# Kernel tuning notes

Measured on AMD Instinct MI355X. Metric: run time of the kernel, lower is better.

## Reference

```python
import jax, jax.numpy as jnp
import numpy as np

B, T, N = 512, 200, 256
ENC_G, ENC_C = 256, 256
C_DIM, G_DIM, U_DIM, F_DIM = 128, 256, 64, 64
CLIP = 5.0


def _gru(x, h, Wih, Whh, bih, bhh):
    # PyTorch nn.GRUCell math
    gi = x @ Wih.T + bih
    gh = h @ Whh.T + bhh
    ir, iz, inn = jnp.split(gi, 3, axis=-1)
    hr, hz, hn = jnp.split(gh, 3, axis=-1)
    r = jax.nn.sigmoid(ir + hr)
    z = jax.nn.sigmoid(iz + hz)
    n = jnp.tanh(inn + r * hn)
    return (1.0 - z) * n + z * h


def setup_inputs() -> dict:
    key = jax.random.key(0)
    ks = iter(jax.random.split(key, 64))

    def gru_p(i, h):
        return (jax.random.normal(next(ks), (3 * h, i)) * i ** -0.5,
                jax.random.normal(next(ks), (3 * h, h)) * h ** -0.5,
                jnp.zeros(3 * h), jnp.zeros(3 * h))

    def lin_p(i, o):
        return (jax.random.normal(next(ks), (o, i)) * i ** -0.5, jnp.zeros(o))

    inp = {}
    inp['x'] = jax.random.uniform(next(ks), (B, T, N))
    inp['eps_g0'] = jax.random.normal(next(ks), (B, G_DIM))
    inp['eps_u'] = jax.random.normal(next(ks), (B, T, U_DIM))
    for name, (i, h) in [('gf', (N, ENC_G)), ('gb', (N, ENC_G)),
                         ('cf', (N, ENC_C)), ('cb', (N, ENC_C)),
                         ('ct', (2 * ENC_C + F_DIM, C_DIM)), ('gn', (U_DIM, G_DIM))]:
        Wih, Whh, bih, bhh = gru_p(i, h)
        inp['Wih_' + name] = Wih; inp['Whh_' + name] = Whh
        inp['bih_' + name] = bih; inp['bhh_' + name] = bhh
    for name, (i, o) in [('g0m', (2 * ENC_G, G_DIM)), ('g0v', (2 * ENC_G, G_DIM)),
                         ('um', (C_DIM, U_DIM)), ('uv', (C_DIM, U_DIM)),
                         ('f', (G_DIM, F_DIM)), ('r', (F_DIM, N))]:
        W, b = lin_p(i, o)
        inp['W_' + name] = W; inp['b_' + name] = b
    return inp


def reference(x, eps_g0, eps_u,
              Wih_gf, Whh_gf, bih_gf, bhh_gf,
              Wih_gb, Whh_gb, bih_gb, bhh_gb,
              Wih_cf, Whh_cf, bih_cf, bhh_cf,
              Wih_cb, Whh_cb, bih_cb, bhh_cb,
              Wih_ct, Whh_ct, bih_ct, bhh_ct,
              Wih_gn, Whh_gn, bih_gn, bhh_gn,
              W_g0m, b_g0m, W_g0v, b_g0v,
              W_um, b_um, W_uv, b_uv,
              W_f, b_f, W_r, b_r):
    Bsz = x.shape[0]
    xs = x.transpose(1, 0, 2)  # [T, B, N]
    zg = jnp.zeros((Bsz, ENC_G), x.dtype)
    zc = jnp.zeros((Bsz, ENC_C), x.dtype)

    def make_enc(pg, pc):
        def step(carry, xt):
            hg, hc = carry
            hg = jnp.minimum(_gru(xt, hg, *pg), CLIP)   # clamp(max=clip_val)
            hc = jnp.minimum(_gru(xt, hc, *pc), CLIP)
            return (hg, hc), hc
        return step

    (hgf, _), hcf = jax.lax.scan(
        make_enc((Wih_gf, Whh_gf, bih_gf, bhh_gf), (Wih_cf, Whh_cf, bih_cf, bhh_cf)),
        (zg, zc), xs)
    (hgb, _), hcb = jax.lax.scan(
        make_enc((Wih_gb, Whh_gb, bih_gb, bhh_gb), (Wih_cb, Whh_cb, bih_cb, bhh_cb)),
        (zg, zc), xs[::-1])
    h_enc_g = jnp.concatenate([hgf, hgb], axis=-1)        # [B, 2*ENC_G]
    h_enc_c = jnp.concatenate([hcf, hcb[::-1]], axis=-1)  # [T, B, 2*ENC_C]

    g0_mean = h_enc_g @ W_g0m.T + b_g0m
    g0_logv = jnp.log(jnp.exp(h_enc_g @ W_g0v.T + b_g0v) + 1e-4)
    g0 = eps_g0 * jnp.exp(0.5 * g0_logv) + g0_mean

    f0 = g0 @ W_f.T + b_f
    hc0 = jnp.zeros((Bsz, C_DIM), x.dtype)

    def gen_step(carry, inp):
        h_c, g, f = carry
        henc_t, eps_t = inp
        cin = jnp.concatenate([henc_t, f], axis=-1)
        h_c = jnp.clip(_gru(cin, h_c, Wih_ct, Whh_ct, bih_ct, bhh_ct), 0.0, CLIP)
        um = h_c @ W_um.T + b_um
        ul = h_c @ W_uv.T + b_uv
        u = eps_t * jnp.exp(0.5 * ul) + um
        g = jnp.clip(_gru(u, g, Wih_gn, Whh_gn, bih_gn, bhh_gn), 0.0, CLIP)
        f = g @ W_f.T + b_f
        return (h_c, g, f), (um, ul, f)

    _, (u_means, u_logvs, factors) = jax.lax.scan(
        gen_step, (hc0, g0, f0), (h_enc_c, eps_u.transpose(1, 0, 2)))
    factors = factors.transpose(1, 0, 2)  # [B, T, F_DIM]
    rates = jnp.exp(jnp.clip(factors @ W_r.T + b_r, -CLIP, CLIP))
    return (g0_mean, g0_logv,
            u_means.transpose(1, 0, 2), u_logvs.transpose(1, 0, 2),
            factors, rates)
```

## Files before the change

### kernel.cpp

```cpp
#include <hip/hip_runtime.h>
#include <hip/hip_bf16.h>
#include <stdint.h>

typedef __bf16 bf16x8 __attribute__((ext_vector_type(8)));
typedef __bf16 bf16x4 __attribute__((ext_vector_type(4)));
typedef float  f32x4  __attribute__((ext_vector_type(4)));
typedef unsigned short u16x8 __attribute__((ext_vector_type(8)));

#define MFMA_B16(A_,B_,C_) __builtin_amdgcn_mfma_f32_16x16x32_bf16((A_),(B_),(C_),0,0,0)

static constexpr int TT = 200;
static constexpr int TC = 25;
static constexpr int NCH = 8;

static __device__ __forceinline__ float sig_f(float x){ return 1.f/(1.f+__expf(-x)); }
static __device__ __forceinline__ float tanh_f(float x){
  float e = __expf(-2.f*fabsf(x));
  float t = (1.f-e)/(1.f+e);
  return x<0.f ? -t : t;
}
static __device__ __forceinline__ float bf2f(unsigned short u){
  union{unsigned int i; float f;} v; v.i = ((unsigned)u)<<16; return v.f;
}
static __device__ __forceinline__ int swz_off(int row, int col_bytes, int strideB){
  return (row*strideB + col_bytes) ^ ((row&7)<<4);
}
static __device__ __forceinline__ bf16x8 lds_rdA(const __bf16* buf, int row, int kt, int lq, int strideB){
  return *(const bf16x8*)((const char*)buf + swz_off(row, kt*64 + lq*16, strideB));
}
static __device__ __forceinline__ void lds_wr(__bf16* buf, int row, int dim, int strideB, float v){
  *(__bf16*)((char*)buf + swz_off(row, dim*2, strideB)) = (__bf16)v;
}
static __device__ __forceinline__ void lds_barrier(){
  asm volatile("s_waitcnt lgkmcnt(0)" ::: "memory");
  __builtin_amdgcn_s_barrier();
}

__global__ void cvt_bf16(const float* __restrict__ s, __bf16* __restrict__ d, int n){
  int i = blockIdx.x*blockDim.x + threadIdx.x;
  int st = gridDim.x*blockDim.x;
  for(; i<n; i+=st) d[i] = (__bf16)s[i];
}

__global__ __launch_bounds__(256) void gi_gemm(const float* __restrict__ x,
                                               const __bf16* __restrict__ Wall,
                                               __bf16* __restrict__ gi, int t0){
  const int tid=threadIdx.x, w=tid>>6, l=tid&63, lr=l&15, lq=l>>4;
  const int cell = blockIdx.y;
  const bool fwd = (cell&1)==0;
  const int m0 = blockIdx.x*64;
  const int tloc = m0>>9, b0 = m0&511;
  const int tabs = fwd ? (t0+tloc) : (TT-1-(t0+tloc));
  const int brow = b0 + w*16 + lr;

  const float* xp = x + (size_t)brow*TT*256 + (size_t)tabs*256 + lq*8;
  bf16x8 a[8];
  #pragma unroll
  for(int kt=0;kt<8;kt++){
    float4 f0 = *(const float4*)(xp + kt*32);
    float4 f1 = *(const float4*)(xp + kt*32 + 4);
    bf16x8 v;
    v[0]=(__bf16)f0.x; v[1]=(__bf16)f0.y; v[2]=(__bf16)f0.z; v[3]=(__bf16)f0.w;
    v[4]=(__bf16)f1.x; v[5]=(__bf16)f1.y; v[6]=(__bf16)f1.z; v[7]=(__bf16)f1.w;
    a[kt]=v;
  }
  const __bf16* Wc = Wall + (size_t)cell*768*256;
  #pragma unroll 1
  for(int nt=0;nt<48;nt++){
    f32x4 acc={};
    const __bf16* bp = Wc + (size_t)(nt*16+lr)*256 + lq*8;
    #pragma unroll
    for(int kt=0;kt<8;kt++)
      acc = MFMA_B16(a[kt], *(const bf16x8*)(bp + kt*32), acc);
    bf16x4 pk;
    pk[0]=(__bf16)acc[0]; pk[1]=(__bf16)acc[1]; pk[2]=(__bf16)acc[2]; pk[3]=(__bf16)acc[3];
    *(bf16x4*)(gi + (((size_t)cell*TC + tloc)*768 + nt*16+lr)*512 + b0 + w*16 + lq*4) = pk;
  }
}

struct EncP{
  const __bf16* whh;
  const float*  bih[4];
  const float*  bhh[4];
  const __bf16* gi;
  __bf16* henc;
  float*  hcar;
  int t0;
};
__global__ __launch_bounds__(512,2) void enc_scan(EncP P){
  const int tid=threadIdx.x, w=tid>>6, l=tid&63, lr=l&15, lq=l>>4;
  const int cell=blockIdx.y, b0=blockIdx.x*16;
  const bool fwd = (cell&1)==0;
  const bool isC = cell>=2;
  const int dim0 = w*32;

  __shared__ __align__(16) __bf16 hA[2][16*256];
  __shared__ __align__(16) __bf16 giL[2][768*16];
  __shared__ float blds[1024];

  for(int d=tid; d<256; d+=512){
    blds[d]     = P.bih[cell][d]     + P.bhh[cell][d];
    blds[256+d] = P.bih[cell][256+d] + P.bhh[cell][256+d];
    blds[512+d] = P.bih[cell][512+d];
    blds[768+d] = P.bhh[cell][512+d];
  }
  bf16x8 wreg[2][3][8];
  {
    const __bf16* Wh = P.whh + (size_t)cell*768*256;
    #pragma unroll
    for(int jt=0;jt<2;jt++)
      #pragma unroll
      for(int g=0;g<3;g++)
        #pragma unroll
        for(int kt=0;kt<8;kt++)
          wreg[jt][g][kt] = *(const bf16x8*)(Wh + (size_t)(g*256 + dim0 + jt*16 + lr)*256 + kt*32 + lq*8);
  }
  f32x4 hold[2];
  #pragma unroll
  for(int jt=0;jt<2;jt++)
    #pragma unroll
    for(int rr=0;rr<4;rr++){
      float v = P.hcar[((size_t)cell*512 + b0 + lq*4+rr)*256 + dim0 + jt*16 + lr];
      hold[jt][rr] = v;
      lds_wr(hA[0], lq*4+rr, dim0+jt*16+lr, 512, v);
    }
  const int prow = w*96 + (l>>1), phal = l&1;
  const __bf16* gbase = P.gi + ((size_t)cell*TC*768 + prow)*512 + b0 + phal*8;
  u16x8 pf0, pf1, pf2;
  pf0 = *(const u16x8*)(gbase + (size_t)0*768*512 +  0*512);
  pf1 = *(const u16x8*)(gbase + (size_t)0*768*512 + 32*512);
  pf2 = *(const u16x8*)(gbase + (size_t)0*768*512 + 64*512);
  __syncthreads();
  {
    __bf16* gl = giL[0] + prow*16 + phal*8;
    *(u16x8*)(gl)        = pf0;
    *(u16x8*)(gl+32*16)  = pf1;
    *(u16x8*)(gl+64*16)  = pf2;
  }
  { int sn = 1 < TC ? 1 : TC-1;
    pf0 = *(const u16x8*)(gbase + (size_t)sn*768*512 +  0*512);
    pf1 = *(const u16x8*)(gbase + (size_t)sn*768*512 + 32*512);
    pf2 = *(const u16x8*)(gbase + (size_t)sn*768*512 + 64*512);
  }
  lds_barrier();

  int p=0, q=0;
  #pragma unroll 1
  for(int s=0;s<TC;s++){
    const int tglob = P.t0 + s;
    const int tx = fwd ? tglob : (TT-1-tglob);
    if(s+1<TC){
      __bf16* gl = giL[1-q] + prow*16 + phal*8;
      *(u16x8*)(gl)        = pf0;
      *(u16x8*)(gl+32*16)  = pf1;
      *(u16x8*)(gl+64*16)  = pf2;
    }
    { int sn = (s+2<TC) ? s+2 : TC-1;
      pf0 = *(const u16x8*)(gbase + (size_t)sn*768*512 +  0*512);
      pf1 = *(const u16x8*)(gbase + (size_t)sn*768*512 + 32*512);
      pf2 = *(const u16x8*)(gbase + (size_t)sn*768*512 + 64*512);
    }
    const __bf16* gq = giL[q];
    #pragma unroll
    for(int jt=0;jt<2;jt++){
      f32x4 aR={}, aZ={}, aH={};
      #pragma unroll
      for(int kt=0;kt<8;kt++){
        bf16x8 frag = lds_rdA(hA[p], lr, kt, lq, 512);
        aR = MFMA_B16(frag, wreg[jt][0][kt], aR);
        aZ = MFMA_B16(frag, wreg[jt][1][kt], aZ);
        aH = MFMA_B16(frag, wreg[jt][2][kt], aH);
      }
      const int d = dim0 + jt*16 + lr;
      ushort4 gR = *(const ushort4*)(gq + (0*256+d)*16 + lq*4);
      ushort4 gZ = *(const ushort4*)(gq + (1*256+d)*16 + lq*4);
      ushort4 gN = *(const ushort4*)(gq + (2*256+d)*16 + lq*4);
      const float bR=blds[d], bZ=blds[256+d], bI=blds[512+d], bH=blds[768+d];
      const unsigned short* uR=(const unsigned short*)&gR;
      const unsigned short* uZ=(const unsigned short*)&gZ;
      const unsigned short* uN=(const unsigned short*)&gN;
      #pragma unroll
      for(int rr=0;rr<4;rr++){
        float r = sig_f(aR[rr] + bf2f(uR[rr]) + bR);
        float z = sig_f(aZ[rr] + bf2f(uZ[rr]) + bZ);
        float nn= tanh_f(bf2f(uN[rr]) + bI + r*(aH[rr] + bH));
        float h = (1.f-z)*nn + z*hold[jt][rr];
        h = fminf(h, 5.f);
        hold[jt][rr] = h;
        lds_wr(hA[1-p], lq*4+rr, d, 512, h);
      }
    }
    if(isC){
      const int row = l>>2, dgrp = (l&3)*8;
      bf16x8 hv = *(const bf16x8*)((const char*)hA[1-p] +
                    ((row*512 + (dim0+dgrp)*2) ^ ((row&7)<<4)));
      *(bf16x8*)(P.henc + ((size_t)tx*512 + b0 + row)*512 + (cell==3?256:0) + dim0 + dgrp) = hv;
    }
    lds_barrier();
    p ^= 1; q ^= 1;
  }
  #pragma unroll
  for(int jt=0;jt<2;jt++)
    #pragma unroll
    for(int rr=0;rr<4;rr++)
      P.hcar[((size_t)cell*512 + b0 + lq*4+rr)*256 + dim0 + jt*16 + lr] = hold[jt][rr];
}

__global__ void g0_kernel(const float* __restrict__ hgf, const float* __restrict__ hgb,
                          const float* __restrict__ Wm, const float* __restrict__ bm,
                          const float* __restrict__ Wv, const float* __restrict__ bv,
                          const float* __restrict__ eps,
                          float* __restrict__ o_mean, float* __restrict__ o_logv,
                          float* __restrict__ g0){
  int j = blockIdx.x*blockDim.x + threadIdx.x;
  int b = j>>8, d = j&255;
  const float4* hf=(const float4*)(hgf + (size_t)b*256);
  const float4* hb=(const float4*)(hgb + (size_t)b*256);
  const float4* mp=(const float4*)(Wm + (size_t)d*512);
  const float4* vp=(const float4*)(Wv + (size_t)d*512);
  float am=0.f, av=0.f;
  #pragma unroll 4
  for(int k=0;k<64;k++){
    float4 h=hf[k], m=mp[k], v=vp[k];
    am += h.x*m.x + h.y*m.y + h.z*m.z + h.w*m.w;
    av += h.x*v.x + h.y*v.y + h.z*v.z + h.w*v.w;
  }
  #pragma unroll 4
  for(int k=0;k<64;k++){
    float4 h=hb[k], m=mp[64+k], v=vp[64+k];
    am += h.x*m.x + h.y*m.y + h.z*m.z + h.w*m.w;
    av += h.x*v.x + h.y*v.y + h.z*v.z + h.w*v.w;
  }
  float mean = am + bm[d];
  float ev   = __expf(av + bv[d]) + 1e-4f;
  float lv   = __logf(ev);
  o_mean[j]=mean; o_logv[j]=lv;
  g0[j] = eps[j]*sqrtf(ev) + mean;
}

__global__ __launch_bounds__(256,2) void gict_gemm(const __bf16* __restrict__ henc,
                                                   const __bf16* __restrict__ wct,
                                                   __bf16* __restrict__ gictT){
  const int tid=threadIdx.x, w=tid>>6, l=tid&63, lr=l&15, lq=l>>4;
  const int m0 = blockIdx.x*8 + w*2;
  bf16x8 a[2][16];
  #pragma unroll
  for(int m=0;m<2;m++){
    const __bf16* ap = henc + (size_t)((m0+m)*16 + lr)*512 + lq*8;
    #pragma unroll
    for(int kt=0;kt<16;kt++) a[m][kt] = *(const bf16x8*)(ap + kt*32);
  }
  #pragma unroll 1
  for(int nt=0;nt<24;nt++){
    f32x4 c0={}, c1={};
    const __bf16* bp = wct + (size_t)(nt*16+lr)*576 + lq*8;
    #pragma unroll
    for(int kt=0;kt<16;kt++){
      bf16x8 bb = *(const bf16x8*)(bp + kt*32);
      c0 = MFMA_B16(a[0][kt], bb, c0);
      c1 = MFMA_B16(a[1][kt], bb, c1);
    }
    #pragma unroll
    for(int m=0;m<2;m++){
      f32x4 c = m? c1 : c0;
      int R0 = (m0+m)*16 + lq*4;
      int t  = R0>>9, b = R0&511;
      bf16x4 pk;
      pk[0]=(__bf16)c[0]; pk[1]=(__bf16)c[1]; pk[2]=(__bf16)c[2]; pk[3]=(__bf16)c[3];
      *(bf16x4*)(gictT + ((size_t)t*384 + nt*16+lr)*512 + b) = pk;
    }
  }
}

struct GenP{
  const __bf16 *wct, *whh_ct, *wih_gn, *whh_gn, *w_um, *w_uv, *w_f;
  const float  *bih_ct, *bhh_ct, *bih_gn, *bhh_gn, *b_um, *b_uv, *b_f;
  const __bf16* gihT;
  const float*  g0;
  const float*  eps_u;
  float *o_um, *o_ul, *o_f;
};
__global__ __launch_bounds__(512,2) void gen_scan(GenP P){
  const int tid=threadIdx.x, w=tid>>6, l=tid&63, lr=l&15, lq=l>>4;
  const int b0 = blockIdx.x*16;

  __shared__ __align__(16) __bf16 wgnL[768*64];
  __shared__ __align__(16) __bf16 hcA[2][16*128];
  __shared__ __align__(16) __bf16 gA [2][16*256];
  __shared__ __align__(16) __bf16 uA [16*64];
  __shared__ __align__(16) __bf16 fA [16*64];

  for(int c=tid; c<6144; c+=512){
    int row = c>>3, part = c&7;
    bf16x8 v = *(const bf16x8*)(P.wih_gn + (size_t)row*64 + part*8);
    *(bf16x8*)((char*)wgnL + ((row*128 + part*16) ^ ((row&7)<<4))) = v;
  }
  bf16x8 wrz[2][2][8];
  #pragma unroll
  for(int jt=0;jt<2;jt++)
    #pragma unroll
    for(int g=0;g<2;g++)
      #pragma unroll
      for(int kt=0;kt<8;kt++)
        wrz[jt][g][kt] = *(const bf16x8*)(P.whh_gn + (size_t)(g*256 + w*32 + jt*16 + lr)*256 + kt*32 + lq*8);

  const int dct = w*16 + lr;
  const int du  = (w&3)*16 + lr;
  const float bctR = P.bih_ct[dct]     + P.bhh_ct[dct];
  const float bctZ = P.bih_ct[128+dct] + P.bhh_ct[128+dct];
  const float bctI = P.bih_ct[256+dct];
  const float bctH = P.bhh_ct[256+dct];
  float bgnR[2], bgnZ[2], bgnI[2], bgnH[2];
  #pragma unroll
  for(int jt=0;jt<2;jt++){
    int d = w*32 + jt*16 + lr;
    bgnR[jt] = P.bih_gn[d]     + P.bhh_gn[d];
    bgnZ[jt] = P.bih_gn[256+d] + P.bhh_gn[256+d];
    bgnI[jt] = P.bih_gn[512+d];
    bgnH[jt] = P.bhh_gn[512+d];
  }
  const float bum = P.b_um[du], buv = P.b_uv[du], bff = P.b_f[du];

  f32x4 gC[2], hcC;
  hcC = (f32x4){};
  #pragma unroll
  for(int jt=0;jt<2;jt++)
    #pragma unroll
    for(int rr=0;rr<4;rr++){
      float v = P.g0[(size_t)(b0+lq*4+rr)*256 + w*32 + jt*16 + lr];
      gC[jt][rr] = v;
      lds_wr(gA[0], lq*4+rr, w*32+jt*16+lr, 512, v);
    }
  for(int i=tid;i<16*128;i+=512) hcA[0][i] = (__bf16)0.f;
  __syncthreads();
  if(w<4){
    f32x4 fa={};
    #pragma unroll
    for(int kt=0;kt<8;kt++){
      bf16x8 gf = lds_rdA(gA[0], lr, kt, lq, 512);
      fa = MFMA_B16(gf, *(const bf16x8*)(P.w_f + (size_t)du*256 + kt*32 + lq*8), fa);
    }
    #pragma unroll
    for(int rr=0;rr<4;rr++) lds_wr(fA, lq*4+rr, du, 128, fa[rr]+bff);
  }
  ushort4 gpR, gpZ, gpN; float epf[4];
  gpR = *(const ushort4*)(P.gihT + ((size_t)0*384 +       dct)*512 + b0 + lq*4);
  gpZ = *(const ushort4*)(P.gihT + ((size_t)0*384 + 128 + dct)*512 + b0 + lq*4);
  gpN = *(const ushort4*)(P.gihT + ((size_t)0*384 + 256 + dct)*512 + b0 + lq*4);
  if(w<4){
    #pragma unroll
    for(int rr=0;rr<4;rr++) epf[rr] = P.eps_u[((size_t)(b0+lq*4+rr)*TT + 0)*64 + du];
  }
  __syncthreads();

  int pc=0, pg=0;
  #pragma unroll 1
  for(int t=0;t<TT;t++){
    {
      bf16x8 ff0 = lds_rdA(fA, lr, 0, lq, 128);
      bf16x8 ff1 = lds_rdA(fA, lr, 1, lq, 128);
      bf16x8 hp0 = lds_rdA(hcA[pc], lr, 0, lq, 256);
      bf16x8 hp1 = lds_rdA(hcA[pc], lr, 1, lq, 256);
      bf16x8 hp2 = lds_rdA(hcA[pc], lr, 2, lq, 256);
      bf16x8 hp3 = lds_rdA(hcA[pc], lr, 3, lq, 256);
      f32x4 aR={}, aZ={}, aI={}, aH={};
      #pragma unroll
      for(int g=0;g<3;g++){
        const __bf16* wif = P.wct    + (size_t)(g*128+dct)*576 + 512 + lq*8;
        const __bf16* whc = P.whh_ct + (size_t)(g*128+dct)*128 + lq*8;
        bf16x8 wf0 = *(const bf16x8*)(wif);
        bf16x8 wf1 = *(const bf16x8*)(wif + 32);
        bf16x8 wh0 = *(const bf16x8*)(whc);
        bf16x8 wh1 = *(const bf16x8*)(whc + 32);
        bf16x8 wh2 = *(const bf16x8*)(whc + 64);
        bf16x8 wh3 = *(const bf16x8*)(whc + 96);
        if(g==0){
          aR = MFMA_B16(ff0,wf0,aR); aR = MFMA_B16(ff1,wf1,aR);
          aR = MFMA_B16(hp0,wh0,aR); aR = MFMA_B16(hp1,wh1,aR);
          aR = MFMA_B16(hp2,wh2,aR); aR = MFMA_B16(hp3,wh3,aR);
        }else if(g==1){
          aZ = MFMA_B16(ff0,wf0,aZ); aZ = MFMA_B16(ff1,wf1,aZ);
          aZ = MFMA_B16(hp0,wh0,aZ); aZ = MFMA_B16(hp1,wh1,aZ);
          aZ = MFMA_B16(hp2,wh2,aZ); aZ = MFMA_B16(hp3,wh3,aZ);
        }else{
          aI = MFMA_B16(ff0,wf0,aI); aI = MFMA_B16(ff1,wf1,aI);
          aH = MFMA_B16(hp0,wh0,aH); aH = MFMA_B16(hp1,wh1,aH);
          aH = MFMA_B16(hp2,wh2,aH); aH = MFMA_B16(hp3,wh3,aH);
        }
      }
      const unsigned short* uR=(const unsigned short*)&gpR;
      const unsigned short* uZ=(const unsigned short*)&gpZ;
      const unsigned short* uN=(const unsigned short*)&gpN;
      #pragma unroll
      for(int rr=0;rr<4;rr++){
        float r = sig_f(aR[rr] + bf2f(uR[rr]) + bctR);
        float z = sig_f(aZ[rr] + bf2f(uZ[rr]) + bctZ);
        float nn= tanh_f(aI[rr] + bf2f(uN[rr]) + bctI + r*(aH[rr] + bctH));
        float h = (1.f-z)*nn + z*hcC[rr];
        h = fminf(fmaxf(h,0.f), 5.f);
        hcC[rr] = h;
        lds_wr(hcA[1-pc], lq*4+rr, dct, 256, h);
      }
    }
    lds_barrier();

    if(w<4){
      bf16x8 hn0 = lds_rdA(hcA[1-pc], lr, 0, lq, 256);
      bf16x8 hn1 = lds_rdA(hcA[1-pc], lr, 1, lq, 256);
      bf16x8 hn2 = lds_rdA(hcA[1-pc], lr, 2, lq, 256);
      bf16x8 hn3 = lds_rdA(hcA[1-pc], lr, 3, lq, 256);
      f32x4 am={}, av={};
      const __bf16* wm = P.w_um + (size_t)du*128 + lq*8;
      const __bf16* wv = P.w_uv + (size_t)du*128 + lq*8;
      am = MFMA_B16(hn0, *(const bf16x8*)(wm   ), am);
      am = MFMA_B16(hn1, *(const bf16x8*)(wm+32), am);
      am = MFMA_B16(hn2, *(const bf16x8*)(wm+64), am);
      am = MFMA_B16(hn3, *(const bf16x8*)(wm+96), am);
      av = MFMA_B16(hn0, *(const bf16x8*)(wv   ), av);
      av = MFMA_B16(hn1, *(const bf16x8*)(wv+32), av);
      av = MFMA_B16(hn2, *(const bf16x8*)(wv+64), av);
      av = MFMA_B16(hn3, *(const bf16x8*)(wv+96), av);
      #pragma unroll
      for(int rr=0;rr<4;rr++){
        const int row = lq*4+rr;
        float um = am[rr] + bum;
        float ul = av[rr] + buv;
        size_t oi = ((size_t)(b0+row)*TT + t)*64 + du;
        P.o_um[oi] = um;
        P.o_ul[oi] = ul;
        float u = epf[rr]*__expf(0.5f*ul) + um;
        lds_wr(uA, row, du, 128, u);
      }
    }
    lds_barrier();

    {
      const int tn = (t+1<TT)? t+1 : TT-1;
      gpR = *(const ushort4*)(P.gihT + ((size_t)tn*384 +       dct)*512 + b0 + lq*4);
      gpZ = *(const ushort4*)(P.gihT + ((size_t)tn*384 + 128 + dct)*512 + b0 + lq*4);
      gpN = *(const ushort4*)(P.gihT + ((size_t)tn*384 + 256 + dct)*512 + b0 + lq*4);
      if(w<4){
        #pragma unroll
        for(int rr=0;rr<4;rr++) epf[rr] = P.eps_u[((size_t)(b0+lq*4+rr)*TT + tn)*64 + du];
      }
      bf16x8 uf0 = lds_rdA(uA, lr, 0, lq, 128);
      bf16x8 uf1 = lds_rdA(uA, lr, 1, lq, 128);
      #pragma unroll
      for(int jt=0;jt<2;jt++){
        const int dg = w*32 + jt*16 + lr;
        bf16x8 wn[8];
        #pragma unroll
        for(int kt=0;kt<8;kt++)
          wn[kt] = *(const bf16x8*)(P.whh_gn + (size_t)(512 + dg)*256 + kt*32 + lq*8);
        f32x4 aR={}, aZ={}, aI={}, aH={};
        #pragma unroll
        for(int g=0;g<3;g++){
          const int row = g*256 + dg;
          bf16x8 w0 = *(const bf16x8*)((const char*)wgnL + ((row*128 +  0 + lq*16) ^ ((row&7)<<4)));
          bf16x8 w1 = *(const bf16x8*)((const char*)wgnL + ((row*128 + 64 + lq*16) ^ ((row&7)<<4)));
          if(g==0){ aR = MFMA_B16(uf0,w0,aR); aR = MFMA_B16(uf1,w1,aR); }
          else if(g==1){ aZ = MFMA_B16(uf0,w0,aZ); aZ = MFMA_B16(uf1,w1,aZ); }
          else { aI = MFMA_B16(uf0,w0,aI); aI = MFMA_B16(uf1,w1,aI); }
        }
        #pragma unroll
        for(int kt=0;kt<8;kt++){
          bf16x8 gf = lds_rdA(gA[pg], lr, kt, lq, 512);
          aR = MFMA_B16(gf, wrz[jt][0][kt], aR);
          aZ = MFMA_B16(gf, wrz[jt][1][kt], aZ);
          aH = MFMA_B16(gf, wn[kt], aH);
        }
        #pragma unroll
        for(int rr=0;rr<4;rr++){
          float r = sig_f(aR[rr] + bgnR[jt]);
          float z = sig_f(aZ[rr] + bgnZ[jt]);
          float nn= tanh_f(aI[rr] + bgnI[jt] + r*(aH[rr] + bgnH[jt]));
          float gv = (1.f-z)*nn + z*gC[jt][rr];
          gv = fminf(fmaxf(gv,0.f), 5.f);
          gC[jt][rr] = gv;
          lds_wr(gA[1-pg], lq*4+rr, dg, 512, gv);
        }
      }
    }
    lds_barrier();

    if(w<4){
      f32x4 fa={};
      const __bf16* wfp = P.w_f + (size_t)du*256 + lq*8;
      #pragma unroll
      for(int kt=0;kt<8;kt++){
        bf16x8 gf = lds_rdA(gA[1-pg], lr, kt, lq, 512);
        fa = MFMA_B16(gf, *(const bf16x8*)(wfp + kt*32), fa);
      }
      #pragma unroll
      for(int rr=0;rr<4;rr++){
        const int row = lq*4+rr;
        float v = fa[rr] + bff;
        P.o_f[((size_t)(b0+row)*TT + t)*64 + du] = v;
        lds_wr(fA, row, du, 128, v);
      }
    }
    lds_barrier();
    pc ^= 1; pg ^= 1;
  }
}

__global__ void rates_k(const float* __restrict__ fac, const float* __restrict__ Wr,
                        const float* __restrict__ br, float* __restrict__ out){
  const int total = 512*200*256;
  int i = blockIdx.x*blockDim.x + threadIdx.x;
  int st = gridDim.x*blockDim.x;
  for(; i<total; i+=st){
    int row = i>>8, n = i&255;
    const float4* fp=(const float4*)(fac + (size_t)row*64);
    const float4* wp=(const float4*)(Wr  + (size_t)n*64);
    float a = 0.f;
    #pragma unroll
    for(int k=0;k<16;k++){
      float4 f=fp[k], ww=wp[k];
      a += f.x*ww.x + f.y*ww.y + f.z*ww.z + f.w*ww.w;
    }
    a += br[n];
    a = fminf(fmaxf(a, -5.f), 5.f);
    out[i] = __expf(a);
  }
}

extern "C" void kernel_launch(void* const* d_in, const int* in_sizes, int n_in,
                              void* d_out, int out_size, void* d_ws, size_t ws_size,
                              hipStream_t stream){
  (void)in_sizes; (void)n_in; (void)out_size; (void)ws_size;
  const float* x      = (const float*)d_in[0];
  const float* eps_g0 = (const float*)d_in[1];
  const float* eps_u  = (const float*)d_in[2];
  const float* Wih_f[6]; const float* Whh_f[6]; const float* bih[6]; const float* bhh[6];
  for(int c=0;c<6;c++){
    Wih_f[c]=(const float*)d_in[3+4*c]; Whh_f[c]=(const float*)d_in[4+4*c];
    bih[c]  =(const float*)d_in[5+4*c]; bhh[c]  =(const float*)d_in[6+4*c];
  }
  const float* W_g0m=(const float*)d_in[27]; const float* b_g0m=(const float*)d_in[28];
  const float* W_g0v=(const float*)d_in[29]; const float* b_g0v=(const float*)d_in[30];
  const float* W_um =(const float*)d_in[31]; const float* b_um =(const float*)d_in[32];
  const float* W_uv =(const float*)d_in[33]; const float* b_uv =(const float*)d_in[34];
  const float* W_f  =(const float*)d_in[35]; const float* b_f  =(const float*)d_in[36];
  const float* W_r  =(const float*)d_in[37]; const float* b_r  =(const float*)d_in[38];

  char* ws = (char*)d_ws; size_t off = 0;
  auto alloc = [&](size_t bytes)->char*{
    char* p = ws + off; off = (off + bytes + 255) & ~(size_t)255; return p;
  };
  __bf16* wencall = (__bf16*)alloc((size_t)4*768*256*2);
  __bf16* whhall  = (__bf16*)alloc((size_t)4*768*256*2);
  __bf16* wct_b   = (__bf16*)alloc((size_t)384*576*2);
  __bf16* whhct_b = (__bf16*)alloc((size_t)384*128*2);
  __bf16* wihgn_b = (__bf16*)alloc((size_t)768*64*2);
  __bf16* whhgn_b = (__bf16*)alloc((size_t)768*256*2);
  __bf16* wum_b   = (__bf16*)alloc((size_t)64*128*2);
  __bf16* wuv_b   = (__bf16*)alloc((size_t)64*128*2);
  __bf16* wf_b    = (__bf16*)alloc((size_t)64*256*2);
  __bf16* henc    = (__bf16*)alloc((size_t)200*512*512*2);
  __bf16* gi_buf  = (__bf16*)alloc((size_t)4*TC*768*512*2);
  float*  hcar    = (float*)alloc((size_t)4*512*256*4);
  float*  g0buf   = (float*)alloc((size_t)512*256*4);

  for(int c=0;c<4;c++){
    cvt_bf16<<<128,256,0,stream>>>(Wih_f[c], wencall + (size_t)c*768*256, 768*256);
    cvt_bf16<<<128,256,0,stream>>>(Whh_f[c], whhall  + (size_t)c*768*256, 768*256);
  }
  cvt_bf16<<<128,256,0,stream>>>(Wih_f[4], wct_b,   384*576);
  cvt_bf16<<<64 ,256,0,stream>>>(Whh_f[4], whhct_b, 384*128);
  cvt_bf16<<<64 ,256,0,stream>>>(Wih_f[5], wihgn_b, 768*64);
  cvt_bf16<<<128,256,0,stream>>>(Whh_f[5], whhgn_b, 768*256);
  cvt_bf16<<<32 ,256,0,stream>>>(W_um, wum_b, 64*128);
  cvt_bf16<<<32 ,256,0,stream>>>(W_uv, wuv_b, 64*128);
  cvt_bf16<<<32 ,256,0,stream>>>(W_f,  wf_b,  64*256);
  hipMemsetAsync(hcar, 0, (size_t)4*512*256*4, stream);

  EncP ep;
  ep.whh = whhall;
  for(int c=0;c<4;c++){ ep.bih[c]=bih[c]; ep.bhh[c]=bhh[c]; }
  ep.gi = gi_buf; ep.henc = henc; ep.hcar = hcar;
  for(int k=0;k<NCH;k++){
    gi_gemm<<<dim3((512*TC)/64,4),256,0,stream>>>(x, wencall, gi_buf, k*TC);
    ep.t0 = k*TC;
    enc_scan<<<dim3(32,4),512,0,stream>>>(ep);
  }

  float* out = (float*)d_out;
  float* o_mean = out;
  float* o_logv = out + 131072;
  float* o_um   = out + 262144;
  float* o_ul   = out + 6815744;
  float* o_f    = out + 13369344;
  float* o_r    = out + 19922944;

  g0_kernel<<<512,256,0,stream>>>(hcar + 0, hcar + (size_t)1*512*256,
                                  W_g0m,b_g0m, W_g0v,b_g0v, eps_g0,
                                  o_mean,o_logv, g0buf);
  gict_gemm<<<800,256,0,stream>>>(henc, wct_b, gi_buf);

  GenP gp;
  gp.wct=wct_b; gp.whh_ct=whhct_b; gp.wih_gn=wihgn_b; gp.whh_gn=whhgn_b;
  gp.w_um=wum_b; gp.w_uv=wuv_b; gp.w_f=wf_b;
  gp.bih_ct=bih[4]; gp.bhh_ct=bhh[4]; gp.bih_gn=bih[5]; gp.bhh_gn=bhh[5];
  gp.b_um=b_um; gp.b_uv=b_uv; gp.b_f=b_f;
  gp.gihT=gi_buf; gp.g0=g0buf; gp.eps_u=eps_u;
  gp.o_um=o_um; gp.o_ul=o_ul; gp.o_f=o_f;
  gen_scan<<<32,512,0,stream>>>(gp);

  rates_k<<<8192,256,0,stream>>>(o_f, W_r, b_r, o_r);
}
```

Measured before the change: 7.137 ms.

## Rebalance register-resident GRU weights and prefetch recurrent weights across barriers

In the encoder scan, only the r and z recurrent weight blocks stay in registers, pinned with an empty asm so the compiler keeps them resident. The n-gate weights are now streamed from global memory each step, which cuts VGPR pressure. In the generator, the controller's hidden-to-hidden weights and the first n-gate tile are loaded before barriers so the loads overlap synchronization. The factor projection moves from waves 0-3 to waves 4-7 so it no longer lands on the same waves as the u projection. This trades extra global or L2 weight traffic per step for fewer spills and better overlap.

Measured after the change: 7.520 ms. +5.4%, slower.

```diff
diff --git a/kernel.cpp b/kernel.cpp
--- a/kernel.cpp
+++ b/kernel.cpp
@@ -22,6 +22,8 @@
 static __device__ __forceinline__ float bf2f(unsigned short u){
   union{unsigned int i; float f;} v; v.i = ((unsigned)u)<<16; return v.f;
 }
+static __device__ __forceinline__ void pin8(bf16x8 &v){ asm volatile("" : "+v"(v)); }
+
 static __device__ __forceinline__ int swz_off(int row, int col_bytes, int strideB){
   return (row*strideB + col_bytes) ^ ((row&7)<<4);
 }
@@ -104,17 +106,17 @@
     blds[512+d] = P.bih[cell][512+d];
     blds[768+d] = P.bhh[cell][512+d];
   }
-  bf16x8 wreg[2][3][8];
-  {
-    const __bf16* Wh = P.whh + (size_t)cell*768*256;
-    #pragma unroll
-    for(int jt=0;jt<2;jt++)
-      #pragma unroll
-      for(int g=0;g<3;g++)
-        #pragma unroll
-        for(int kt=0;kt<8;kt++)
-          wreg[jt][g][kt] = *(const bf16x8*)(Wh + (size_t)(g*256 + dim0 + jt*16 + lr)*256 + kt*32 + lq*8);
-  }
+  const __bf16* Wh = P.whh + (size_t)cell*768*256;
+  bf16x8 wreg[2][2][8];
+  #pragma unroll
+  for(int jt=0;jt<2;jt++)
+    #pragma unroll
+    for(int g=0;g<2;g++)
+      #pragma unroll
+      for(int kt=0;kt<8;kt++){
+        wreg[jt][g][kt] = *(const bf16x8*)(Wh + (size_t)(g*256 + dim0 + jt*16 + lr)*256 + kt*32 + lq*8);
+        pin8(wreg[jt][g][kt]);
+      }
   f32x4 hold[2];
   #pragma unroll
   for(int jt=0;jt<2;jt++)
@@ -163,15 +165,16 @@
     const __bf16* gq = giL[q];
     #pragma unroll
     for(int jt=0;jt<2;jt++){
+      const int d = dim0 + jt*16 + lr;
+      const __bf16* whN = Wh + (size_t)(512 + d)*256 + lq*8;
       f32x4 aR={}, aZ={}, aH={};
       #pragma unroll
       for(int kt=0;kt<8;kt++){
         bf16x8 frag = lds_rdA(hA[p], lr, kt, lq, 512);
         aR = MFMA_B16(frag, wreg[jt][0][kt], aR);
         aZ = MFMA_B16(frag, wreg[jt][1][kt], aZ);
-        aH = MFMA_B16(frag, wreg[jt][2][kt], aH);
-      }
-      const int d = dim0 + jt*16 + lr;
+        aH = MFMA_B16(frag, *(const bf16x8*)(whN + kt*32), aH);
+      }
       ushort4 gR = *(const ushort4*)(gq + (0*256+d)*16 + lq*4);
       ushort4 gZ = *(const ushort4*)(gq + (1*256+d)*16 + lq*4);
       ushort4 gN = *(const ushort4*)(gq + (2*256+d)*16 + lq*4);
@@ -301,11 +304,14 @@
     #pragma unroll
     for(int g=0;g<2;g++)
       #pragma unroll
-      for(int kt=0;kt<8;kt++)
+      for(int kt=0;kt<8;kt++){
         wrz[jt][g][kt] = *(const bf16x8*)(P.whh_gn + (size_t)(g*256 + w*32 + jt*16 + lr)*256 + kt*32 + lq*8);
+        pin8(wrz[jt][g][kt]);
+      }
 
   const int dct = w*16 + lr;
-  const int du  = (w&3)*16 + lr;
+  const int duu = (w&3)*16 + lr;
+  const int duf = (w&3)*16 + lr;
   const float bctR = P.bih_ct[dct]     + P.bhh_ct[dct];
   const float bctZ = P.bih_ct[128+dct] + P.bhh_ct[128+dct];
   const float bctI = P.bih_ct[256+dct];
@@ -319,7 +325,7 @@
     bgnI[jt] = P.bih_gn[512+d];
     bgnH[jt] = P.bhh_gn[512+d];
   }
-  const float bum = P.b_um[du], buv = P.b_uv[du], bff = P.b_f[du];
+  const float bum = P.b_um[duu], buv = P.b_uv[duu], bff = P.b_f[duf];
 
   f32x4 gC[2], hcC;
   hcC = (f32x4){};
@@ -333,15 +339,15 @@
     }
   for(int i=tid;i<16*128;i+=512) hcA[0][i] = (__bf16)0.f;
   __syncthreads();
-  if(w<4){
+  if(w>=4){
     f32x4 fa={};
     #pragma unroll
     for(int kt=0;kt<8;kt++){
       bf16x8 gf = lds_rdA(gA[0], lr, kt, lq, 512);
-      fa = MFMA_B16(gf, *(const bf16x8*)(P.w_f + (size_t)du*256 + kt*32 + lq*8), fa);
-    }
-    #pragma unroll
-    for(int rr=0;rr<4;rr++) lds_wr(fA, lq*4+rr, du, 128, fa[rr]+bff);
+      fa = MFMA_B16(gf, *(const bf16x8*)(P.w_f + (size_t)duf*256 + kt*32 + lq*8), fa);
+    }
+    #pragma unroll
+    for(int rr=0;rr<4;rr++) lds_wr(fA, lq*4+rr, duf, 128, fa[rr]+bff);
   }
   ushort4 gpR, gpZ, gpN; float epf[4];
   gpR = *(const ushort4*)(P.gihT + ((size_t)0*384 +       dct)*512 + b0 + lq*4);
@@ -349,8 +355,14 @@
   gpN = *(const ushort4*)(P.gihT + ((size_t)0*384 + 256 + dct)*512 + b0 + lq*4);
   if(w<4){
     #pragma unroll
-    for(int rr=0;rr<4;rr++) epf[rr] = P.eps_u[((size_t)(b0+lq*4+rr)*TT + 0)*64 + du];
-  }
+    for(int rr=0;rr<4;rr++) epf[rr] = P.eps_u[((size_t)(b0+lq*4+rr)*TT + 0)*64 + duu];
+  }
+  bf16x8 cwh[3][4];
+  #pragma unroll
+  for(int g=0;g<3;g++)
+    #pragma unroll
+    for(int kt=0;kt<4;kt++)
+      cwh[g][kt] = *(const bf16x8*)(P.whh_ct + (size_t)(g*128+dct)*128 + kt*32 + lq*8);
   __syncthreads();
 
   int pc=0, pg=0;
@@ -366,26 +378,21 @@
       f32x4 aR={}, aZ={}, aI={}, aH={};
       #pragma unroll
       for(int g=0;g<3;g++){
-        const __bf16* wif = P.wct    + (size_t)(g*128+dct)*576 + 512 + lq*8;
-        const __bf16* whc = P.whh_ct + (size_t)(g*128+dct)*128 + lq*8;
+        const __bf16* wif = P.wct + (size_t)(g*128+dct)*576 + 512 + lq*8;
         bf16x8 wf0 = *(const bf16x8*)(wif);
         bf16x8 wf1 = *(const bf16x8*)(wif + 32);
-        bf16x8 wh0 = *(const bf16x8*)(whc);
-        bf16x8 wh1 = *(const bf16x8*)(whc + 32);
-        bf16x8 wh2 = *(const bf16x8*)(whc + 64);
-        bf16x8 wh3 = *(const bf16x8*)(whc + 96);
         if(g==0){
           aR = MFMA_B16(ff0,wf0,aR); aR = MFMA_B16(ff1,wf1,aR);
-          aR = MFMA_B16(hp0,wh0,aR); aR = MFMA_B16(hp1,wh1,aR);
-          aR = MFMA_B16(hp2,wh2,aR); aR = MFMA_B16(hp3,wh3,aR);
+          aR = MFMA_B16(hp0,cwh[0][0],aR); aR = MFMA_B16(hp1,cwh[0][1],aR);
+          aR = MFMA_B16(hp2,cwh[0][2],aR); aR = MFMA_B16(hp3,cwh[0][3],aR);
         }else if(g==1){
           aZ = MFMA_B16(ff0,wf0,aZ); aZ = MFMA_B16(ff1,wf1,aZ);
-          aZ = MFMA_B16(hp0,wh0,aZ); aZ = MFMA_B16(hp1,wh1,aZ);
-          aZ = MFMA_B16(hp2,wh2,aZ); aZ = MFMA_B16(hp3,wh3,aZ);
+          aZ = MFMA_B16(hp0,cwh[1][0],aZ); aZ = MFMA_B16(hp1,cwh[1][1],aZ);
+          aZ = MFMA_B16(hp2,cwh[1][2],aZ); aZ = MFMA_B16(hp3,cwh[1][3],aZ);
         }else{
           aI = MFMA_B16(ff0,wf0,aI); aI = MFMA_B16(ff1,wf1,aI);
-          aH = MFMA_B16(hp0,wh0,aH); aH = MFMA_B16(hp1,wh1,aH);
-          aH = MFMA_B16(hp2,wh2,aH); aH = MFMA_B16(hp3,wh3,aH);
+          aH = MFMA_B16(hp0,cwh[2][0],aH); aH = MFMA_B16(hp1,cwh[2][1],aH);
+          aH = MFMA_B16(hp2,cwh[2][2],aH); aH = MFMA_B16(hp3,cwh[2][3],aH);
         }
       }
       const unsigned short* uR=(const unsigned short*)&gpR;
@@ -410,8 +417,8 @@
       bf16x8 hn2 = lds_rdA(hcA[1-pc], lr, 2, lq, 256);
       bf16x8 hn3 = lds_rdA(hcA[1-pc], lr, 3, lq, 256);
       f32x4 am={}, av={};
-      const __bf16* wm = P.w_um + (size_t)du*128 + lq*8;
-      const __bf16* wv = P.w_uv + (size_t)du*128 + lq*8;
+      const __bf16* wm = P.w_um + (size_t)duu*128 + lq*8;
+      const __bf16* wv = P.w_uv + (size_t)duu*128 + lq*8;
       am = MFMA_B16(hn0, *(const bf16x8*)(wm   ), am);
       am = MFMA_B16(hn1, *(const bf16x8*)(wm+32), am);
       am = MFMA_B16(hn2, *(const bf16x8*)(wm+64), am);
@@ -425,13 +432,17 @@
         const int row = lq*4+rr;
         float um = am[rr] + bum;
         float ul = av[rr] + buv;
-        size_t oi = ((size_t)(b0+row)*TT + t)*64 + du;
+        size_t oi = ((size_t)(b0+row)*TT + t)*64 + duu;
         P.o_um[oi] = um;
         P.o_ul[oi] = ul;
         float u = epf[rr]*__expf(0.5f*ul) + um;
-        lds_wr(uA, row, du, 128, u);
-      }
-    }
+        lds_wr(uA, row, duu, 128, u);
+      }
+    }
+    bf16x8 wn0[8];
+    #pragma unroll
+    for(int kt=0;kt<8;kt++)
+      wn0[kt] = *(const bf16x8*)(P.whh_gn + (size_t)(512 + w*32 + lr)*256 + kt*32 + lq*8);
     lds_barrier();
 
     {
@@ -441,7 +452,7 @@
       gpN = *(const ushort4*)(P.gihT + ((size_t)tn*384 + 256 + dct)*512 + b0 + lq*4);
       if(w<4){
         #pragma unroll
-        for(int rr=0;rr<4;rr++) epf[rr] = P.eps_u[((size_t)(b0+lq*4+rr)*TT + tn)*64 + du];
+        for(int rr=0;rr<4;rr++) epf[rr] = P.eps_u[((size_t)(b0+lq*4+rr)*TT + tn)*64 + duu];
       }
       bf16x8 uf0 = lds_rdA(uA, lr, 0, lq, 128);
       bf16x8 uf1 = lds_rdA(uA, lr, 1, lq, 128);
@@ -449,9 +460,14 @@
       for(int jt=0;jt<2;jt++){
         const int dg = w*32 + jt*16 + lr;
         bf16x8 wn[8];
-        #pragma unroll
-        for(int kt=0;kt<8;kt++)
-          wn[kt] = *(const bf16x8*)(P.whh_gn + (size_t)(512 + dg)*256 + kt*32 + lq*8);
+        if(jt==0){
+          #pragma unroll
+          for(int kt=0;kt<8;kt++) wn[kt] = wn0[kt];
+        }else{
+          #pragma unroll
+          for(int kt=0;kt<8;kt++)
+            wn[kt] = *(const bf16x8*)(P.whh_gn + (size_t)(512 + dg)*256 + kt*32 + lq*8);
+        }
         f32x4 aR={}, aZ={}, aI={}, aH={};
         #pragma unroll
         for(int g=0;g<3;g++){
@@ -483,9 +499,9 @@
     }
     lds_barrier();
 
-    if(w<4){
+    if(w>=4){
       f32x4 fa={};
-      const __bf16* wfp = P.w_f + (size_t)du*256 + lq*8;
+      const __bf16* wfp = P.w_f + (size_t)duf*256 + lq*8;
       #pragma unroll
       for(int kt=0;kt<8;kt++){
         bf16x8 gf = lds_rdA(gA[1-pg], lr, kt, lq, 512);
@@ -495,10 +511,15 @@
       for(int rr=0;rr<4;rr++){
         const int row = lq*4+rr;
         float v = fa[rr] + bff;
-        P.o_f[((size_t)(b0+row)*TT + t)*64 + du] = v;
-        lds_wr(fA, row, du, 128, v);
-      }
-    }
+        P.o_f[((size_t)(b0+row)*TT + t)*64 + duf] = v;
+        lds_wr(fA, row, duf, 128, v);
+      }
+    }
+    #pragma unroll
+    for(int g=0;g<3;g++)
+      #pragma unroll
+      for(int kt=0;kt<4;kt++)
+        cwh[g][kt] = *(const bf16x8*)(P.whh_ct + (size_t)(g*128+dct)*128 + kt*32 + lq*8);
     lds_barrier();
     pc ^= 1; pg ^= 1;
   }
```
